# Kernel optimization log

Measured on AMD Instinct MI355X. Metric: run time of the kernel, lower is better.

Reference implementation:

```python
import jax, jax.numpy as jnp
import numpy as np

DIM = 20
N = 200000
E = 6400000
ITERATIONS = 3


def setup_inputs() -> dict:
    key = jax.random.key(0)
    ks = jax.random.split(key, 20)
    inp = {
        "h": jax.random.normal(ks[0], (N, DIM), dtype=jnp.float32),
        "node2depth": jax.random.randint(ks[1], (N,), 0, 5, dtype=jnp.int32),
        "edge_src": jax.random.randint(ks[2], (E,), 0, N, dtype=jnp.int32),
        "edge_dst": jax.random.randint(ks[3], (E,), 0, N, dtype=jnp.int32),
    }
    # Six DIM x DIM Linear layers (weight stored [out,in] like torch, plus bias)
    scale = 1.0 / np.sqrt(DIM)
    names = ["Wz", "Uz", "Wr", "Ur", "Wh", "Uh"]
    for j, nm in enumerate(names):
        inp[nm + "_w"] = jax.random.uniform(ks[4 + 2 * j], (DIM, DIM), jnp.float32, -scale, scale)
        inp[nm + "_b"] = jax.random.uniform(ks[5 + 2 * j], (DIM,), jnp.float32, -scale, scale)
    return inp


def _linear(x, w, b):
    return x @ w.T + b


def reference(h, Wz_w, Wz_b, Uz_w, Uz_b, Wr_w, Wr_b, Ur_w, Ur_b,
              Wh_w, Wh_b, Uh_w, Uh_b, node2depth, edge_src, edge_dst):
    active = None
    for i in range(ITERATIONS):
        # active set shrinks as i grows (depth + i <= ITERATIONS)
        active = (node2depth + i) <= ITERATIONS  # [N] bool
        af = active.astype(h.dtype)
        # x[u] = sum over neighbors v of h[v], counting only active src AND active dst
        msg = h[edge_src] * af[edge_src][:, None]          # [E, DIM]
        x = jax.ops.segment_sum(msg, edge_dst, num_segments=N)  # [N, DIM]
        x = x * af[:, None]
        z = jax.nn.sigmoid(_linear(x, Wz_w, Wz_b) + _linear(h, Uz_w, Uz_b))
        r = jax.nn.sigmoid(_linear(x, Wr_w, Wr_b) + _linear(h, Ur_w, Ur_b))
        h_cand = jnp.tanh(_linear(x, Wh_w, Wh_b) + _linear(r * h, Uh_w, Uh_b))
        h_new = z * h + (1.0 - z) * h_cand
        # inactive nodes are dropped from the dict in the original; since the
        # active set only shrinks, keeping their old h is equivalent
        h = jnp.where(active[:, None], h_new, h)
    # original returns only nodes active at the last iteration; zero out the rest
    return jnp.where(active[:, None], h, jnp.zeros_like(h))
```

## Files before the change

kernel.cpp:

```cpp
#include <hip/hip_runtime.h>

#define DIM    20
#define NN     200000
#define EE     6400000
#define ITERS  3
#define BLOCK  256

#define NODES_PER_FINE   64
#define NFINE            3125
#define NCOARSE          98
#define FINE_PER_COARSE  32
#define TILE             4096
#define IPT              16

typedef unsigned int u32;

__global__ __launch_bounds__(BLOCK) void k1_count(const int* __restrict__ edst,
                                                  int* __restrict__ fine_cnt) {
    __shared__ u32 lhist[NFINE];
    int tid = threadIdx.x;
    for (int i = tid; i < NFINE; i += BLOCK) lhist[i] = 0;
    __syncthreads();
    for (int e = blockIdx.x * BLOCK + tid; e < EE; e += gridDim.x * BLOCK) {
        int d = edst[e];
        atomicAdd(&lhist[d >> 6], 1u);
    }
    __syncthreads();
    for (int i = tid; i < NFINE; i += BLOCK) {
        u32 v = lhist[i];
        if (v) atomicAdd((u32*)&fine_cnt[i], v);
    }
}

__global__ __launch_bounds__(BLOCK) void k2_scan(const int* __restrict__ fine_cnt,
                                                 int* __restrict__ fine_base,
                                                 int* __restrict__ fine_cursor,
                                                 int* __restrict__ coarse_base,
                                                 int* __restrict__ coarse_cursor) {
    const int CH = 13;
    int tid = threadIdx.x;
    int loc[CH];
    int base = tid * CH;
    int s = 0;
    #pragma unroll
    for (int j = 0; j < CH; ++j) {
        int idx = base + j;
        int v = (idx < NFINE) ? fine_cnt[idx] : 0;
        loc[j] = v; s += v;
    }
    __shared__ int wsum[4];
    int lane = tid & 63, wid = tid >> 6;
    int incl = s;
    #pragma unroll
    for (int off = 1; off < 64; off <<= 1) {
        int t = __shfl_up(incl, off, 64);
        if (lane >= off) incl += t;
    }
    if (lane == 63) wsum[wid] = incl;
    __syncthreads();
    int woff = 0;
    for (int w = 0; w < wid; ++w) woff += wsum[w];
    int run = woff + incl - s;
    #pragma unroll
    for (int j = 0; j < CH; ++j) {
        int idx = base + j;
        if (idx < NFINE) {
            fine_base[idx]   = run;
            fine_cursor[idx] = run;
            run += loc[j];
        }
    }
    if (tid == 0) fine_base[NFINE] = EE;
    __syncthreads();
    if (tid < NCOARSE + 1) {
        int f = tid * FINE_PER_COARSE; if (f > NFINE) f = NFINE;
        int v = fine_base[f];
        coarse_base[tid] = v;
        if (tid < NCOARSE) coarse_cursor[tid] = v;
    }
}

__global__ __launch_bounds__(BLOCK) void p1_split(const int* __restrict__ esrc,
                                                  const int* __restrict__ edst,
                                                  const int* __restrict__ depth,
                                                  int* __restrict__ coarse_cursor,
                                                  u32* __restrict__ buf1) {
    __shared__ u32 lhist[NCOARSE];
    __shared__ u32 gbase[NCOARSE];
    int tid = threadIdx.x;
    int start = blockIdx.x * TILE;
    if (tid < NCOARSE) lhist[tid] = 0;
    __syncthreads();

    u32 item[IPT]; u32 key[IPT]; u32 rank[IPT];
    #pragma unroll
    for (int k = 0; k < IPT; ++k) {
        int e = start + k * BLOCK + tid;
        if (e < EE) {
            int d = edst[e];
            int s = esrc[e];
            u32 dep = (u32)depth[s];
            u32 c = (u32)d >> 11;
            key[k]  = c;
            item[k] = ((u32)d & 2047u) | ((u32)s << 11) | (dep << 29);
            rank[k] = atomicAdd(&lhist[c], 1u);
        }
    }
    __syncthreads();
    if (tid < NCOARSE) {
        u32 cnt = lhist[tid];
        gbase[tid] = cnt ? (u32)atomicAdd((u32*)&coarse_cursor[tid], cnt) : 0u;
    }
    __syncthreads();
    #pragma unroll
    for (int k = 0; k < IPT; ++k) {
        int e = start + k * BLOCK + tid;
        if (e < EE) buf1[gbase[key[k]] + rank[k]] = item[k];
    }
}

__global__ __launch_bounds__(BLOCK) void p2_split(const u32* __restrict__ buf1,
                                                  const int* __restrict__ coarse_base,
                                                  int* __restrict__ fine_cursor,
                                                  u32* __restrict__ buf2) {
    __shared__ u32 lhist[2 * FINE_PER_COARSE];
    __shared__ u32 gbase[2 * FINE_PER_COARSE];
    __shared__ int cb[NCOARSE + 1];
    __shared__ int sc0;
    int tid = threadIdx.x;
    int start = blockIdx.x * TILE;
    if (tid < NCOARSE + 1) cb[tid] = coarse_base[tid];
    if (tid < 2 * FINE_PER_COARSE) { lhist[tid] = 0; gbase[tid] = 0; }
    __syncthreads();
    if (tid == 0) {
        int c = 0;
        while (c + 1 < NCOARSE && cb[c + 1] <= start) ++c;
        sc0 = c;
    }
    __syncthreads();
    int c0 = sc0;
    int b1 = cb[c0 + 1];

    u32 item[IPT]; u32 key[IPT]; u32 rank[IPT];
    #pragma unroll
    for (int k = 0; k < IPT; ++k) {
        int i = start + k * BLOCK + tid;
        if (i < EE) {
            u32 w = buf1[i];
            u32 dlow = w & 2047u;
            u32 sdep = w >> 11;
            u32 kk = ((i < b1) ? 0u : (u32)FINE_PER_COARSE) + (dlow >> 6);
            key[k]  = kk;
            item[k] = (dlow & 63u) | (sdep << 6);
            rank[k] = atomicAdd(&lhist[kk], 1u);
        }
    }
    __syncthreads();
    if (tid < 2 * FINE_PER_COARSE) {
        u32 cnt = lhist[tid];
        int idx = c0 * FINE_PER_COARSE + tid;
        if (cnt && idx < NFINE)
            gbase[tid] = (u32)atomicAdd((u32*)&fine_cursor[idx], cnt);
    }
    __syncthreads();
    #pragma unroll
    for (int k = 0; k < IPT; ++k) {
        int i = start + k * BLOCK + tid;
        if (i < EE) buf2[gbase[key[k]] + rank[k]] = item[k];
    }
}

__global__ __launch_bounds__(BLOCK) void pb_sort(const u32* __restrict__ buf2,
                                                 const int* __restrict__ fine_base,
                                                 int* __restrict__ ptr,
                                                 u32* __restrict__ cnt3,
                                                 u32* __restrict__ ssrc) {
    __shared__ u32 hist[512];
    __shared__ u32 ebase[512];
    __shared__ u32 lout[TILE];
    __shared__ u32 wsum[4];
    int tid = threadIdx.x;
    int b = blockIdx.x;
    int lo = fine_base[b];
    int hi = fine_base[b + 1];
    int cnt = hi - lo;
    hist[tid] = 0; hist[tid + 256] = 0;
    __syncthreads();

    u32 item[IPT]; u32 key[IPT]; u32 rank[IPT];
    #pragma unroll
    for (int k = 0; k < IPT; ++k) {
        int i = lo + k * BLOCK + tid;
        if (i < hi) {
            u32 w = buf2[i];
            u32 kk = (w & 63u) * 8u + (w >> 24);
            key[k]  = kk;
            item[k] = (w >> 6) & 0x3FFFFu;
            rank[k] = atomicAdd(&hist[kk], 1u);
        }
    }
    __syncthreads();
    {
        u32 s0 = hist[2 * tid], s1 = hist[2 * tid + 1];
        u32 s = s0 + s1;
        int lane = tid & 63, wid = tid >> 6;
        u32 incl = s;
        #pragma unroll
        for (int off = 1; off < 64; off <<= 1) {
            u32 t = __shfl_up((int)incl, off, 64);
            if (lane >= off) incl += t;
        }
        if (lane == 63) wsum[wid] = incl;
        __syncthreads();
        u32 woff = 0;
        for (int w = 0; w < wid; ++w) woff += wsum[w];
        u32 excl = woff + incl - s;
        ebase[2 * tid]     = excl;
        ebase[2 * tid + 1] = excl + s0;
    }
    __syncthreads();
    if (tid < NODES_PER_FINE) {
        u32 base0 = ebase[tid * 8];
        u32 c1 = ebase[tid * 8 + 2] - base0;
        u32 c2 = ebase[tid * 8 + 3] - base0;
        u32 c3 = ebase[tid * 8 + 4] - base0;
        int u = b * NODES_PER_FINE + tid;
        ptr[u]  = lo + (int)base0;
        cnt3[u] = c1 | (c2 << 10) | (c3 << 20);
    }
    #pragma unroll
    for (int k = 0; k < IPT; ++k) {
        int i = lo + k * BLOCK + tid;
        if (i < hi) lout[ebase[key[k]] + rank[k]] = item[k];
    }
    __syncthreads();
    for (int j = tid; j < cnt; j += BLOCK) ssrc[lo + j] = lout[j];
}

__device__ __forceinline__ u32 pack_bf16x2(float a, float b) {
    u32 ua = __float_as_uint(a);
    u32 ub = __float_as_uint(b);
    ua = (ua + 0x7FFFu + ((ua >> 16) & 1u)) >> 16;
    ub = (ub + 0x7FFFu + ((ub >> 16) & 1u)) & 0xFFFF0000u;
    return ua | ub;
}

__global__ __launch_bounds__(BLOCK) void hconv(const float* __restrict__ h,
                                               u32* __restrict__ hb) {
    int g = blockIdx.x * BLOCK + threadIdx.x;
    if (g >= NN * 16) return;
    int node = g >> 4, slot = g & 15;
    u32 v = 0;
    if (slot < 10) {
        float2 f = *(const float2*)(h + (size_t)node * DIM + slot * 2);
        v = pack_bf16x2(f.x, f.y);
    }
    hb[g] = v;
}


__device__ __forceinline__ float bl(u32 w) { return __uint_as_float(w << 16); }
__device__ __forceinline__ float bh(u32 w) { return __uint_as_float(w & 0xFFFF0000u); }

__device__ __forceinline__ void acc_bf16row(float* x, uint4 A, uint4 B, uint2 C) {
    x[0]+=bl(A.x);  x[1]+=bh(A.x);  x[2]+=bl(A.y);  x[3]+=bh(A.y);
    x[4]+=bl(A.z);  x[5]+=bh(A.z);  x[6]+=bl(A.w);  x[7]+=bh(A.w);
    x[8]+=bl(B.x);  x[9]+=bh(B.x);  x[10]+=bl(B.y); x[11]+=bh(B.y);
    x[12]+=bl(B.z); x[13]+=bh(B.z); x[14]+=bl(B.w); x[15]+=bh(B.w);
    x[16]+=bl(C.x); x[17]+=bh(C.x); x[18]+=bl(C.y); x[19]+=bh(C.y);
}

__global__ __launch_bounds__(BLOCK) void gather4(
    const u32* __restrict__ hb_in, const int* __restrict__ depth,
    const int* __restrict__ ptr, const u32* __restrict__ cnt3,
    const u32* __restrict__ ssrc, float* __restrict__ xbuf,
    int it, int shift)
{
    int gid = blockIdx.x * BLOCK + threadIdx.x;
    int u = gid >> 2;
    int t = threadIdx.x & 3;
    if (u >= NN) return;
    int lim = ITERS - it;
    if (depth[u] > lim) return;

    int p = ptr[u];
    int d = (int)((cnt3[u] >> shift) & 1023u);

    float x[DIM];
    #pragma unroll
    for (int k = 0; k < DIM; ++k) x[k] = 0.0f;

    int e = t;
    for (; e + 4 < d; e += 8) {
        u32 v0 = ssrc[p + e];
        u32 v1 = ssrc[p + e + 4];
        const u32* r0 = hb_in + (size_t)v0 * 16;
        const u32* r1 = hb_in + (size_t)v1 * 16;
        uint4 A0 = *(const uint4*)r0; uint4 B0 = *(const uint4*)(r0 + 4);
        uint2 C0 = *(const uint2*)(r0 + 8);
        uint4 A1 = *(const uint4*)r1; uint4 B1 = *(const uint4*)(r1 + 4);
        uint2 C1 = *(const uint2*)(r1 + 8);
        acc_bf16row(x, A0, B0, C0);
        acc_bf16row(x, A1, B1, C1);
    }
    if (e < d) {
        u32 v0 = ssrc[p + e];
        const u32* r0 = hb_in + (size_t)v0 * 16;
        uint4 A0 = *(const uint4*)r0; uint4 B0 = *(const uint4*)(r0 + 4);
        uint2 C0 = *(const uint2*)(r0 + 8);
        acc_bf16row(x, A0, B0, C0);
    }

    #pragma unroll
    for (int k = 0; k < DIM; ++k) {
        x[k] += __shfl_xor(x[k], 1, 64);
        x[k] += __shfl_xor(x[k], 2, 64);
    }

    float* xr = xbuf + (size_t)u * DIM;
    #pragma unroll
    for (int q = 0; q < 5; ++q) xr[q * 4 + t] = x[q * 4 + t];
}


__device__ __forceinline__ float fast_sigmoid(float t) {
    return 1.0f / (1.0f + __expf(-t));
}
__device__ __forceinline__ float fast_tanh(float t) {
    t = fminf(fmaxf(t, -15.0f), 15.0f);
    float e2 = __expf(2.0f * t);
    return (e2 - 1.0f) / (e2 + 1.0f);
}

__global__ __launch_bounds__(BLOCK) void gru_node(
    const float* __restrict__ h_in, float* __restrict__ h_out,
    u32* __restrict__ hb_out,
    const int* __restrict__ depth, const float* __restrict__ xbuf,
    const float* __restrict__ Wz, const float* __restrict__ bWz,
    const float* __restrict__ Uz, const float* __restrict__ bUz,
    const float* __restrict__ Wr, const float* __restrict__ bWr,
    const float* __restrict__ Ur, const float* __restrict__ bUr,
    const float* __restrict__ Wh, const float* __restrict__ bWh,
    const float* __restrict__ Uh, const float* __restrict__ bUh,
    int it, int isFinal)
{
    int u = blockIdx.x * BLOCK + threadIdx.x;
    if (u >= NN) return;
    int lim = ITERS - it;
    bool act = depth[u] <= lim;
    if (!act) {
        if (isFinal) {
            float4 z4 = make_float4(0.f, 0.f, 0.f, 0.f);
            float4* o4 = (float4*)(h_out + (size_t)u * DIM);
            #pragma unroll
            for (int q = 0; q < 5; ++q) o4[q] = z4;
        }
        return;
    }

    float x[DIM], h[DIM];
    {
        const float4* xv = (const float4*)(xbuf + (size_t)u * DIM);
        float4 a0 = xv[0], a1 = xv[1], a2 = xv[2], a3 = xv[3], a4 = xv[4];
        x[0]=a0.x; x[1]=a0.y; x[2]=a0.z; x[3]=a0.w;
        x[4]=a1.x; x[5]=a1.y; x[6]=a1.z; x[7]=a1.w;
        x[8]=a2.x; x[9]=a2.y; x[10]=a2.z; x[11]=a2.w;
        x[12]=a3.x; x[13]=a3.y; x[14]=a3.z; x[15]=a3.w;
        x[16]=a4.x; x[17]=a4.y; x[18]=a4.z; x[19]=a4.w;
    }
    {
        const float4* hv = (const float4*)(h_in + (size_t)u * DIM);
        float4 a0 = hv[0], a1 = hv[1], a2 = hv[2], a3 = hv[3], a4 = hv[4];
        h[0]=a0.x; h[1]=a0.y; h[2]=a0.z; h[3]=a0.w;
        h[4]=a1.x; h[5]=a1.y; h[6]=a1.z; h[7]=a1.w;
        h[8]=a2.x; h[9]=a2.y; h[10]=a2.z; h[11]=a2.w;
        h[12]=a3.x; h[13]=a3.y; h[14]=a3.z; h[15]=a3.w;
        h[16]=a4.x; h[17]=a4.y; h[18]=a4.z; h[19]=a4.w;
    }

    float z[DIM], rh[DIM];
    #pragma unroll
    for (int j = 0; j < DIM; ++j) {
        float sz = bWz[j] + bUz[j];
        float sr = bWr[j] + bUr[j];
        #pragma unroll
        for (int k = 0; k < DIM; ++k) {
            sz += x[k] * Wz[j * DIM + k];
            sz += h[k] * Uz[j * DIM + k];
            sr += x[k] * Wr[j * DIM + k];
            sr += h[k] * Ur[j * DIM + k];
        }
        z[j]  = fast_sigmoid(sz);
        rh[j] = fast_sigmoid(sr) * h[j];
    }

    float o[DIM];
    #pragma unroll
    for (int j = 0; j < DIM; ++j) {
        float sh = bWh[j] + bUh[j];
        #pragma unroll
        for (int k = 0; k < DIM; ++k) {
            sh += x[k]  * Wh[j * DIM + k];
            sh += rh[k] * Uh[j * DIM + k];
        }
        float hc = fast_tanh(sh);
        o[j] = z[j] * h[j] + (1.0f - z[j]) * hc;
    }

    {
        float4* o4 = (float4*)(h_out + (size_t)u * DIM);
        o4[0] = make_float4(o[0],  o[1],  o[2],  o[3]);
        o4[1] = make_float4(o[4],  o[5],  o[6],  o[7]);
        o4[2] = make_float4(o[8],  o[9],  o[10], o[11]);
        o4[3] = make_float4(o[12], o[13], o[14], o[15]);
        o4[4] = make_float4(o[16], o[17], o[18], o[19]);
    }
    if (!isFinal) {
        u32* row = hb_out + (size_t)u * 16;
        uint4 wA = make_uint4(pack_bf16x2(o[0], o[1]),  pack_bf16x2(o[2], o[3]),
                              pack_bf16x2(o[4], o[5]),  pack_bf16x2(o[6], o[7]));
        uint4 wB = make_uint4(pack_bf16x2(o[8], o[9]),  pack_bf16x2(o[10], o[11]),
                              pack_bf16x2(o[12], o[13]), pack_bf16x2(o[14], o[15]));
        uint2 wC = make_uint2(pack_bf16x2(o[16], o[17]), pack_bf16x2(o[18], o[19]));
        *(uint4*)row       = wA;
        *(uint4*)(row + 4) = wB;
        *(uint2*)(row + 8) = wC;
    }
}


extern "C" void kernel_launch(void* const* d_in, const int* in_sizes, int n_in,
                              void* d_out, int out_size, void* d_ws, size_t ws_size,
                              hipStream_t stream) {
    const float* h0    = (const float*)d_in[0];
    const int*   depth = (const int*)d_in[1];
    const int*   esrc  = (const int*)d_in[2];
    const int*   edst  = (const int*)d_in[3];
    const float* Wz  = (const float*)d_in[4];  const float* bWz = (const float*)d_in[5];
    const float* Uz  = (const float*)d_in[6];  const float* bUz = (const float*)d_in[7];
    const float* Wr  = (const float*)d_in[8];  const float* bWr = (const float*)d_in[9];
    const float* Ur  = (const float*)d_in[10]; const float* bUr = (const float*)d_in[11];
    const float* Wh  = (const float*)d_in[12]; const float* bWh = (const float*)d_in[13];
    const float* Uh  = (const float*)d_in[14]; const float* bUh = (const float*)d_in[15];
    float* out = (float*)d_out;

    int* W = (int*)d_ws;
    int*  fine_cnt      = W + 0;
    int*  fine_base     = W + 3200;
    int*  fine_cursor   = W + 6400;
    int*  coarse_base   = W + 9600;
    int*  coarse_cursor = W + 9728;
    int*  ptr           = W + 9856;
    u32*  cnt3          = (u32*)(W + 209920);
    u32*  buf1          = (u32*)(W + 409984);
    u32*  buf2          = buf1 + EE;
    float* h1           = (float*)(buf2 + EE);
    u32*  hbA           = (u32*)(h1 + (size_t)NN * DIM);
    u32*  hbB           = hbA + (size_t)NN * 16;
    float* xbuf         = (float*)(hbB + (size_t)NN * 16);
    u32*  ssrc          = buf1;
    float* h2           = (float*)buf2;

    hipMemsetAsync(fine_cnt, 0, NFINE * sizeof(int), stream);

    int ntile = (EE + TILE - 1) / TILE;
    int ngrid = (NN + BLOCK - 1) / BLOCK;
    int ggrid = (NN * 4) / BLOCK;

    k1_count<<<256, BLOCK, 0, stream>>>(edst, fine_cnt);
    k2_scan <<<1,   BLOCK, 0, stream>>>(fine_cnt, fine_base, fine_cursor,
                                        coarse_base, coarse_cursor);
    p1_split<<<ntile, BLOCK, 0, stream>>>(esrc, edst, depth, coarse_cursor, buf1);
    p2_split<<<ntile, BLOCK, 0, stream>>>(buf1, coarse_base, fine_cursor, buf2);
    pb_sort <<<NFINE, BLOCK, 0, stream>>>(buf2, fine_base, ptr, cnt3, ssrc);
    hconv   <<<(NN * 16) / BLOCK, BLOCK, 0, stream>>>(h0, hbA);

    gather4 <<<ggrid, BLOCK, 0, stream>>>(hbA, depth, ptr, cnt3, ssrc, xbuf, 0, 20);
    gru_node<<<ngrid, BLOCK, 0, stream>>>(h0, h1, hbB, depth, xbuf,
        Wz, bWz, Uz, bUz, Wr, bWr, Ur, bUr, Wh, bWh, Uh, bUh, 0, 0);
    gather4 <<<ggrid, BLOCK, 0, stream>>>(hbB, depth, ptr, cnt3, ssrc, xbuf, 1, 10);
    gru_node<<<ngrid, BLOCK, 0, stream>>>(h1, h2, hbA, depth, xbuf,
        Wz, bWz, Uz, bUz, Wr, bWr, Ur, bUr, Wh, bWh, Uh, bUh, 1, 0);
    gather4 <<<ggrid, BLOCK, 0, stream>>>(hbA, depth, ptr, cnt3, ssrc, xbuf, 2, 0);
    gru_node<<<ngrid, BLOCK, 0, stream>>>(h2, out, hbB, depth, xbuf,
        Wz, bWz, Uz, bUz, Wr, bWr, Ur, bUr, Wh, bWh, Uh, bUh, 2, 1);
}
```

Before: 553.9 us.

## Split GRU node update across four lanes per node with shared-memory staged stores

The GRU kernel now assigns four threads to each node, each computing five of the twenty output features. The r*h vector is exchanged between the four lanes with wave shuffles. Results are staged in shared memory so the fp32 and bf16 rows can be written with coalesced stores. The aim is to cut per-thread register pressure and serial FMA depth and to improve occupancy and store coalescing, at the cost of a block barrier, extra shuffles and some redundant reads of x and h.

```diff
diff --git a/kernel.cpp b/kernel.cpp
--- a/kernel.cpp
+++ b/kernel.cpp
@@ -332,7 +332,7 @@
     return (e2 - 1.0f) / (e2 + 1.0f);
 }
 
-__global__ __launch_bounds__(BLOCK) void gru_node(
+__global__ __launch_bounds__(BLOCK, 6) void gru_node4(
     const float* __restrict__ h_in, float* __restrict__ h_out,
     u32* __restrict__ hb_out,
     const int* __restrict__ depth, const float* __restrict__ xbuf,
@@ -344,87 +344,108 @@
     const float* __restrict__ Uh, const float* __restrict__ bUh,
     int it, int isFinal)
 {
-    int u = blockIdx.x * BLOCK + threadIdx.x;
-    if (u >= NN) return;
+    __shared__ float xl[64 * DIM];
+    int tid = threadIdx.x;
+    int nl  = tid >> 2;
+    int t   = tid & 3;
+    int j0  = t * 5;
+    int u   = blockIdx.x * 64 + nl;
     int lim = ITERS - it;
     bool act = depth[u] <= lim;
-    if (!act) {
-        if (isFinal) {
-            float4 z4 = make_float4(0.f, 0.f, 0.f, 0.f);
-            float4* o4 = (float4*)(h_out + (size_t)u * DIM);
+
+    if (act) {
+        float az[5], ar[5], ah[5];
+        #pragma unroll
+        for (int jj = 0; jj < 5; ++jj) {
+            az[jj] = bWz[j0 + jj] + bUz[j0 + jj];
+            ar[jj] = bWr[j0 + jj] + bUr[j0 + jj];
+            ah[jj] = bWh[j0 + jj] + bUh[j0 + jj];
+        }
+
+        {
+            float x[DIM];
+            const float4* xv = (const float4*)(xbuf + (size_t)u * DIM);
             #pragma unroll
-            for (int q = 0; q < 5; ++q) o4[q] = z4;
-        }
-        return;
-    }
-
-    float x[DIM], h[DIM];
-    {
-        const float4* xv = (const float4*)(xbuf + (size_t)u * DIM);
-        float4 a0 = xv[0], a1 = xv[1], a2 = xv[2], a3 = xv[3], a4 = xv[4];
-        x[0]=a0.x; x[1]=a0.y; x[2]=a0.z; x[3]=a0.w;
-        x[4]=a1.x; x[5]=a1.y; x[6]=a1.z; x[7]=a1.w;
-        x[8]=a2.x; x[9]=a2.y; x[10]=a2.z; x[11]=a2.w;
-        x[12]=a3.x; x[13]=a3.y; x[14]=a3.z; x[15]=a3.w;
-        x[16]=a4.x; x[17]=a4.y; x[18]=a4.z; x[19]=a4.w;
-    }
-    {
-        const float4* hv = (const float4*)(h_in + (size_t)u * DIM);
-        float4 a0 = hv[0], a1 = hv[1], a2 = hv[2], a3 = hv[3], a4 = hv[4];
-        h[0]=a0.x; h[1]=a0.y; h[2]=a0.z; h[3]=a0.w;
-        h[4]=a1.x; h[5]=a1.y; h[6]=a1.z; h[7]=a1.w;
-        h[8]=a2.x; h[9]=a2.y; h[10]=a2.z; h[11]=a2.w;
-        h[12]=a3.x; h[13]=a3.y; h[14]=a3.z; h[15]=a3.w;
-        h[16]=a4.x; h[17]=a4.y; h[18]=a4.z; h[19]=a4.w;
-    }
-
-    float z[DIM], rh[DIM];
-    #pragma unroll
-    for (int j = 0; j < DIM; ++j) {
-        float sz = bWz[j] + bUz[j];
-        float sr = bWr[j] + bUr[j];
+            for (int q = 0; q < 5; ++q) {
+                float4 v = xv[q];
+                x[q*4] = v.x; x[q*4+1] = v.y; x[q*4+2] = v.z; x[q*4+3] = v.w;
+            }
+            #pragma unroll
+            for (int jj = 0; jj < 5; ++jj) {
+                const float* wz = Wz + (size_t)(j0 + jj) * DIM;
+                const float* wr = Wr + (size_t)(j0 + jj) * DIM;
+                const float* wh = Wh + (size_t)(j0 + jj) * DIM;
+                #pragma unroll
+                for (int k = 0; k < DIM; ++k) {
+                    az[jj] += x[k] * wz[k];
+                    ar[jj] += x[k] * wr[k];
+                    ah[jj] += x[k] * wh[k];
+                }
+            }
+        }
+
+        float zz[5], rh[5], hmine[5];
+        {
+            float h[DIM];
+            const float4* hv = (const float4*)(h_in + (size_t)u * DIM);
+            #pragma unroll
+            for (int q = 0; q < 5; ++q) {
+                float4 v = hv[q];
+                h[q*4] = v.x; h[q*4+1] = v.y; h[q*4+2] = v.z; h[q*4+3] = v.w;
+            }
+            #pragma unroll
+            for (int jj = 0; jj < 5; ++jj) {
+                const float* uz = Uz + (size_t)(j0 + jj) * DIM;
+                const float* ur = Ur + (size_t)(j0 + jj) * DIM;
+                float sz = az[jj], sr = ar[jj];
+                #pragma unroll
+                for (int k = 0; k < DIM; ++k) {
+                    sz += h[k] * uz[k];
+                    sr += h[k] * ur[k];
+                }
+                zz[jj]    = fast_sigmoid(sz);
+                rh[jj]    = fast_sigmoid(sr) * h[j0 + jj];
+                hmine[jj] = h[j0 + jj];
+            }
+        }
+
+        float rh_all[DIM];
+        int baselane = (tid & 63) & ~3;
         #pragma unroll
-        for (int k = 0; k < DIM; ++k) {
-            sz += x[k] * Wz[j * DIM + k];
-            sz += h[k] * Uz[j * DIM + k];
-            sr += x[k] * Wr[j * DIM + k];
-            sr += h[k] * Ur[j * DIM + k];
-        }
-        z[j]  = fast_sigmoid(sz);
-        rh[j] = fast_sigmoid(sr) * h[j];
-    }
-
-    float o[DIM];
-    #pragma unroll
-    for (int j = 0; j < DIM; ++j) {
-        float sh = bWh[j] + bUh[j];
+        for (int tt = 0; tt < 4; ++tt) {
+            #pragma unroll
+            for (int i = 0; i < 5; ++i)
+                rh_all[tt * 5 + i] = __shfl(rh[i], baselane + tt, 64);
+        }
+
         #pragma unroll
-        for (int k = 0; k < DIM; ++k) {
-            sh += x[k]  * Wh[j * DIM + k];
-            sh += rh[k] * Uh[j * DIM + k];
-        }
-        float hc = fast_tanh(sh);
-        o[j] = z[j] * h[j] + (1.0f - z[j]) * hc;
-    }
-
-    {
-        float4* o4 = (float4*)(h_out + (size_t)u * DIM);
-        o4[0] = make_float4(o[0],  o[1],  o[2],  o[3]);
-        o4[1] = make_float4(o[4],  o[5],  o[6],  o[7]);
-        o4[2] = make_float4(o[8],  o[9],  o[10], o[11]);
-        o4[3] = make_float4(o[12], o[13], o[14], o[15]);
-        o4[4] = make_float4(o[16], o[17], o[18], o[19]);
+        for (int jj = 0; jj < 5; ++jj) {
+            const float* uh = Uh + (size_t)(j0 + jj) * DIM;
+            float sh = ah[jj];
+            #pragma unroll
+            for (int k = 0; k < DIM; ++k) sh += rh_all[k] * uh[k];
+            float hc = fast_tanh(sh);
+            xl[nl * DIM + j0 + jj] = zz[jj] * hmine[jj] + (1.0f - zz[jj]) * hc;
+        }
+    } else if (isFinal) {
+        #pragma unroll
+        for (int i = 0; i < 5; ++i) xl[nl * DIM + j0 + i] = 0.0f;
+    }
+    __syncthreads();
+
+    int nb = blockIdx.x * 64;
+    for (int i = tid; i < 64 * 5; i += BLOCK) {
+        int node = i / 5, seg = i - node * 5;
+        const float* s = xl + node * DIM + seg * 4;
+        float4 v = make_float4(s[0], s[1], s[2], s[3]);
+        ((float4*)(h_out + (size_t)(nb + node) * DIM))[seg] = v;
     }
     if (!isFinal) {
-        u32* row = hb_out + (size_t)u * 16;
-        uint4 wA = make_uint4(pack_bf16x2(o[0], o[1]),  pack_bf16x2(o[2], o[3]),
-                              pack_bf16x2(o[4], o[5]),  pack_bf16x2(o[6], o[7]));
-        uint4 wB = make_uint4(pack_bf16x2(o[8], o[9]),  pack_bf16x2(o[10], o[11]),
-                              pack_bf16x2(o[12], o[13]), pack_bf16x2(o[14], o[15]));
-        uint2 wC = make_uint2(pack_bf16x2(o[16], o[17]), pack_bf16x2(o[18], o[19]));
-        *(uint4*)row       = wA;
-        *(uint4*)(row + 4) = wB;
-        *(uint2*)(row + 8) = wC;
+        for (int i = tid; i < 64 * 10; i += BLOCK) {
+            int node = i / 10, d = i - node * 10;
+            const float* s = xl + node * DIM + d * 2;
+            hb_out[(size_t)(nb + node) * 16 + d] = pack_bf16x2(s[0], s[1]);
+        }
     }
 }
 
@@ -464,8 +485,8 @@
     hipMemsetAsync(fine_cnt, 0, NFINE * sizeof(int), stream);
 
     int ntile = (EE + TILE - 1) / TILE;
-    int ngrid = (NN + BLOCK - 1) / BLOCK;
     int ggrid = (NN * 4) / BLOCK;
+    int ugrid = NN / 64;
 
     k1_count<<<256, BLOCK, 0, stream>>>(edst, fine_cnt);
     k2_scan <<<1,   BLOCK, 0, stream>>>(fine_cnt, fine_base, fine_cursor,
@@ -475,13 +496,13 @@
     pb_sort <<<NFINE, BLOCK, 0, stream>>>(buf2, fine_base, ptr, cnt3, ssrc);
     hconv   <<<(NN * 16) / BLOCK, BLOCK, 0, stream>>>(h0, hbA);
 
-    gather4 <<<ggrid, BLOCK, 0, stream>>>(hbA, depth, ptr, cnt3, ssrc, xbuf, 0, 20);
-    gru_node<<<ngrid, BLOCK, 0, stream>>>(h0, h1, hbB, depth, xbuf,
+    gather4  <<<ggrid, BLOCK, 0, stream>>>(hbA, depth, ptr, cnt3, ssrc, xbuf, 0, 20);
+    gru_node4<<<ugrid, BLOCK, 0, stream>>>(h0, h1, hbB, depth, xbuf,
         Wz, bWz, Uz, bUz, Wr, bWr, Ur, bUr, Wh, bWh, Uh, bUh, 0, 0);
-    gather4 <<<ggrid, BLOCK, 0, stream>>>(hbB, depth, ptr, cnt3, ssrc, xbuf, 1, 10);
-    gru_node<<<ngrid, BLOCK, 0, stream>>>(h1, h2, hbA, depth, xbuf,
+    gather4  <<<ggrid, BLOCK, 0, stream>>>(hbB, depth, ptr, cnt3, ssrc, xbuf, 1, 10);
+    gru_node4<<<ugrid, BLOCK, 0, stream>>>(h1, h2, hbA, depth, xbuf,
         Wz, bWz, Uz, bUz, Wr, bWr, Ur, bUr, Wh, bWh, Uh, bUh, 1, 0);
-    gather4 <<<ggrid, BLOCK, 0, stream>>>(hbA, depth, ptr, cnt3, ssrc, xbuf, 2, 0);
-    gru_node<<<ngrid, BLOCK, 0, stream>>>(h2, out, hbB, depth, xbuf,
+    gather4  <<<ggrid, BLOCK, 0, stream>>>(hbA, depth, ptr, cnt3, ssrc, xbuf, 2, 0);
+    gru_node4<<<ugrid, BLOCK, 0, stream>>>(h2, out, hbB, depth, xbuf,
         Wz, bWz, Uz, bUz, Wr, bWr, Ur, bUr, Wh, bWh, Uh, bUh, 2, 1);
 }
```

Result: slower. 718.2 us (+29.6%).

## Fuse neighbor gather and GRU update into one per-iteration kernel

Applied to the files above, without the earlier changes.

Merges the gather kernel and the GRU node kernel into a single kernel per iteration. Each block of 256 threads gathers neighbor sums for 64 nodes into shared memory, then 64 threads run the GRU update. This removes the global xbuf round trip and three kernel launches. In exchange, only one wavefront per block does the GRU math while the other three idle, which lowers occupancy during that phase.

```diff
diff --git a/kernel.cpp b/kernel.cpp
--- a/kernel.cpp
+++ b/kernel.cpp
@@ -12,6 +12,7 @@
 #define FINE_PER_COARSE  32
 #define TILE             4096
 #define IPT              16
+#define XSTRIDE          21
 
 typedef unsigned int u32;
 
@@ -270,59 +271,6 @@
     x[16]+=bl(C.x); x[17]+=bh(C.x); x[18]+=bl(C.y); x[19]+=bh(C.y);
 }
 
-__global__ __launch_bounds__(BLOCK) void gather4(
-    const u32* __restrict__ hb_in, const int* __restrict__ depth,
-    const int* __restrict__ ptr, const u32* __restrict__ cnt3,
-    const u32* __restrict__ ssrc, float* __restrict__ xbuf,
-    int it, int shift)
-{
-    int gid = blockIdx.x * BLOCK + threadIdx.x;
-    int u = gid >> 2;
-    int t = threadIdx.x & 3;
-    if (u >= NN) return;
-    int lim = ITERS - it;
-    if (depth[u] > lim) return;
-
-    int p = ptr[u];
-    int d = (int)((cnt3[u] >> shift) & 1023u);
-
-    float x[DIM];
-    #pragma unroll
-    for (int k = 0; k < DIM; ++k) x[k] = 0.0f;
-
-    int e = t;
-    for (; e + 4 < d; e += 8) {
-        u32 v0 = ssrc[p + e];
-        u32 v1 = ssrc[p + e + 4];
-        const u32* r0 = hb_in + (size_t)v0 * 16;
-        const u32* r1 = hb_in + (size_t)v1 * 16;
-        uint4 A0 = *(const uint4*)r0; uint4 B0 = *(const uint4*)(r0 + 4);
-        uint2 C0 = *(const uint2*)(r0 + 8);
-        uint4 A1 = *(const uint4*)r1; uint4 B1 = *(const uint4*)(r1 + 4);
-        uint2 C1 = *(const uint2*)(r1 + 8);
-        acc_bf16row(x, A0, B0, C0);
-        acc_bf16row(x, A1, B1, C1);
-    }
-    if (e < d) {
-        u32 v0 = ssrc[p + e];
-        const u32* r0 = hb_in + (size_t)v0 * 16;
-        uint4 A0 = *(const uint4*)r0; uint4 B0 = *(const uint4*)(r0 + 4);
-        uint2 C0 = *(const uint2*)(r0 + 8);
-        acc_bf16row(x, A0, B0, C0);
-    }
-
-    #pragma unroll
-    for (int k = 0; k < DIM; ++k) {
-        x[k] += __shfl_xor(x[k], 1, 64);
-        x[k] += __shfl_xor(x[k], 2, 64);
-    }
-
-    float* xr = xbuf + (size_t)u * DIM;
-    #pragma unroll
-    for (int q = 0; q < 5; ++q) xr[q * 4 + t] = x[q * 4 + t];
-}
-
-
 __device__ __forceinline__ float fast_sigmoid(float t) {
     return 1.0f / (1.0f + __expf(-t));
 }
@@ -332,21 +280,67 @@
     return (e2 - 1.0f) / (e2 + 1.0f);
 }
 
-__global__ __launch_bounds__(BLOCK) void gru_node(
+__global__ __launch_bounds__(BLOCK) void grnn_iter(
     const float* __restrict__ h_in, float* __restrict__ h_out,
-    u32* __restrict__ hb_out,
-    const int* __restrict__ depth, const float* __restrict__ xbuf,
+    const u32* __restrict__ hb_in, u32* __restrict__ hb_out,
+    const int* __restrict__ depth, const int* __restrict__ ptr,
+    const u32* __restrict__ cnt3, const u32* __restrict__ ssrc,
     const float* __restrict__ Wz, const float* __restrict__ bWz,
     const float* __restrict__ Uz, const float* __restrict__ bUz,
     const float* __restrict__ Wr, const float* __restrict__ bWr,
     const float* __restrict__ Ur, const float* __restrict__ bUr,
     const float* __restrict__ Wh, const float* __restrict__ bWh,
     const float* __restrict__ Uh, const float* __restrict__ bUh,
-    int it, int isFinal)
+    int it, int shift, int isFinal)
 {
-    int u = blockIdx.x * BLOCK + threadIdx.x;
-    if (u >= NN) return;
+    __shared__ float xl[64 * XSTRIDE];
+    int tid = threadIdx.x;
+    int nl  = tid >> 2;
+    int t   = tid & 3;
     int lim = ITERS - it;
+
+    {
+        int u = blockIdx.x * 64 + nl;
+        if (depth[u] <= lim) {
+            int p = ptr[u];
+            int d = (int)((cnt3[u] >> shift) & 1023u);
+            float x[DIM];
+            #pragma unroll
+            for (int k = 0; k < DIM; ++k) x[k] = 0.0f;
+            int e = t;
+            for (; e + 4 < d; e += 8) {
+                u32 v0 = ssrc[p + e];
+                u32 v1 = ssrc[p + e + 4];
+                const u32* r0 = hb_in + (size_t)v0 * 16;
+                const u32* r1 = hb_in + (size_t)v1 * 16;
+                uint4 A0 = *(const uint4*)r0; uint4 B0 = *(const uint4*)(r0 + 4);
+                uint2 C0 = *(const uint2*)(r0 + 8);
+                uint4 A1 = *(const uint4*)r1; uint4 B1 = *(const uint4*)(r1 + 4);
+                uint2 C1 = *(const uint2*)(r1 + 8);
+                acc_bf16row(x, A0, B0, C0);
+                acc_bf16row(x, A1, B1, C1);
+            }
+            if (e < d) {
+                u32 v0 = ssrc[p + e];
+                const u32* r0 = hb_in + (size_t)v0 * 16;
+                uint4 A0 = *(const uint4*)r0; uint4 B0 = *(const uint4*)(r0 + 4);
+                uint2 C0 = *(const uint2*)(r0 + 8);
+                acc_bf16row(x, A0, B0, C0);
+            }
+            #pragma unroll
+            for (int k = 0; k < DIM; ++k) {
+                x[k] += __shfl_xor(x[k], 1, 64);
+                x[k] += __shfl_xor(x[k], 2, 64);
+            }
+            float* xr = xl + nl * XSTRIDE;
+            #pragma unroll
+            for (int q = 0; q < 5; ++q) xr[q * 4 + t] = x[q * 4 + t];
+        }
+    }
+    __syncthreads();
+    if (tid >= 64) return;
+
+    int u = blockIdx.x * 64 + tid;
     bool act = depth[u] <= lim;
     if (!act) {
         if (isFinal) {
@@ -359,15 +353,8 @@
     }
 
     float x[DIM], h[DIM];
-    {
-        const float4* xv = (const float4*)(xbuf + (size_t)u * DIM);
-        float4 a0 = xv[0], a1 = xv[1], a2 = xv[2], a3 = xv[3], a4 = xv[4];
-        x[0]=a0.x; x[1]=a0.y; x[2]=a0.z; x[3]=a0.w;
-        x[4]=a1.x; x[5]=a1.y; x[6]=a1.z; x[7]=a1.w;
-        x[8]=a2.x; x[9]=a2.y; x[10]=a2.z; x[11]=a2.w;
-        x[12]=a3.x; x[13]=a3.y; x[14]=a3.z; x[15]=a3.w;
-        x[16]=a4.x; x[17]=a4.y; x[18]=a4.z; x[19]=a4.w;
-    }
+    #pragma unroll
+    for (int k = 0; k < DIM; ++k) x[k] = xl[tid * XSTRIDE + k];
     {
         const float4* hv = (const float4*)(h_in + (size_t)u * DIM);
         float4 a0 = hv[0], a1 = hv[1], a2 = hv[2], a3 = hv[3], a4 = hv[4];
@@ -457,15 +444,12 @@
     float* h1           = (float*)(buf2 + EE);
     u32*  hbA           = (u32*)(h1 + (size_t)NN * DIM);
     u32*  hbB           = hbA + (size_t)NN * 16;
-    float* xbuf         = (float*)(hbB + (size_t)NN * 16);
     u32*  ssrc          = buf1;
     float* h2           = (float*)buf2;
 
     hipMemsetAsync(fine_cnt, 0, NFINE * sizeof(int), stream);
 
     int ntile = (EE + TILE - 1) / TILE;
-    int ngrid = (NN + BLOCK - 1) / BLOCK;
-    int ggrid = (NN * 4) / BLOCK;
 
     k1_count<<<256, BLOCK, 0, stream>>>(edst, fine_cnt);
     k2_scan <<<1,   BLOCK, 0, stream>>>(fine_cnt, fine_base, fine_cursor,
@@ -475,13 +459,10 @@
     pb_sort <<<NFINE, BLOCK, 0, stream>>>(buf2, fine_base, ptr, cnt3, ssrc);
     hconv   <<<(NN * 16) / BLOCK, BLOCK, 0, stream>>>(h0, hbA);
 
-    gather4 <<<ggrid, BLOCK, 0, stream>>>(hbA, depth, ptr, cnt3, ssrc, xbuf, 0, 20);
-    gru_node<<<ngrid, BLOCK, 0, stream>>>(h0, h1, hbB, depth, xbuf,
-        Wz, bWz, Uz, bUz, Wr, bWr, Ur, bUr, Wh, bWh, Uh, bUh, 0, 0);
-    gather4 <<<ggrid, BLOCK, 0, stream>>>(hbB, depth, ptr, cnt3, ssrc, xbuf, 1, 10);
-    gru_node<<<ngrid, BLOCK, 0, stream>>>(h1, h2, hbA, depth, xbuf,
-        Wz, bWz, Uz, bUz, Wr, bWr, Ur, bUr, Wh, bWh, Uh, bUh, 1, 0);
-    gather4 <<<ggrid, BLOCK, 0, stream>>>(hbA, depth, ptr, cnt3, ssrc, xbuf, 2, 0);
-    gru_node<<<ngrid, BLOCK, 0, stream>>>(h2, out, hbB, depth, xbuf,
-        Wz, bWz, Uz, bUz, Wr, bWr, Ur, bUr, Wh, bWh, Uh, bUh, 2, 1);
-}
+    grnn_iter<<<NFINE, BLOCK, 0, stream>>>(h0, h1, hbA, hbB, depth, ptr, cnt3, ssrc,
+        Wz, bWz, Uz, bUz, Wr, bWr, Ur, bUr, Wh, bWh, Uh, bUh, 0, 20, 0);
+    grnn_iter<<<NFINE, BLOCK, 0, stream>>>(h1, h2, hbB, hbA, depth, ptr, cnt3, ssrc,
+        Wz, bWz, Uz, bUz, Wr, bWr, Ur, bUr, Wh, bWh, Uh, bUh, 1, 10, 0);
+    grnn_iter<<<NFINE, BLOCK, 0, stream>>>(h2, out, hbA, hbB, depth, ptr, cnt3, ssrc,
+        Wz, bWz, Uz, bUz, Wr, bWr, Ur, bUr, Wh, bWh, Uh, bUh, 2, 0, 1);
+}
```

New measurement: 515.7 us. 1.07x faster.
